# Optimization experiments

Hardware: AMD Instinct MI355X
Metric: run time of the kernel (lower is better)

Reference implementation:

```python
import jax, jax.numpy as jnp
import numpy as np

B, L, T = 64, 128, 48
E, HE, H = 512, 1024, 1024


def setup_inputs() -> dict:
    key = jax.random.key(0)
    ks = jax.random.split(key, 20)
    s = 0.02
    inp = {
        'enc_hiddens': jax.random.normal(ks[0], (B, L, HE), jnp.float32),
        'enc_masks': jax.random.randint(ks[1], (B, L), 0, 2, jnp.int32),
        'h1_init': jax.random.normal(ks[2], (B, H), jnp.float32),
        'c1_init': jax.random.normal(ks[3], (B, H), jnp.float32),
        'h2_init': jax.random.normal(ks[4], (B, H), jnp.float32),
        'c2_init': jax.random.normal(ks[5], (B, H), jnp.float32),
        'captions': jax.random.normal(ks[6], (T, B, E), jnp.float32),
        # LSTMCell 1: input E -> hidden H
        'W_ih1': jax.random.normal(ks[7], (4 * H, E), jnp.float32) * s,
        'W_hh1': jax.random.normal(ks[8], (4 * H, H), jnp.float32) * s,
        'b_ih1': jnp.zeros((4 * H,), jnp.float32),
        'b_hh1': jnp.zeros((4 * H,), jnp.float32),
        # LSTMCell 2: input 2H -> hidden H
        'W_ih2': jax.random.normal(ks[9], (4 * H, 2 * H), jnp.float32) * s,
        'W_hh2': jax.random.normal(ks[10], (4 * H, H), jnp.float32) * s,
        'b_ih2': jnp.zeros((4 * H,), jnp.float32),
        'b_hh2': jnp.zeros((4 * H,), jnp.float32),
        # att_projection: He -> H
        'W_att': jax.random.normal(ks[11], (H, HE), jnp.float32) * s,
        'b_att': jnp.zeros((H,), jnp.float32),
        # combined_output_projection: He+H -> H
        'W_comb': jax.random.normal(ks[12], (H, HE + H), jnp.float32) * s,
        'b_comb': jnp.zeros((H,), jnp.float32),
    }
    return inp


def _lstm_cell(x, h, c, W_ih, W_hh, b_ih, b_hh):
    gates = x @ W_ih.T + b_ih + h @ W_hh.T + b_hh  # (B, 4H)
    i, f, g, o = jnp.split(gates, 4, axis=-1)
    i = jax.nn.sigmoid(i)
    f = jax.nn.sigmoid(f)
    g = jnp.tanh(g)
    o = jax.nn.sigmoid(o)
    c_new = f * c + i * g
    h_new = o * jnp.tanh(c_new)
    return h_new, c_new


def reference(enc_hiddens, enc_masks, h1_init, c1_init, h2_init, c2_init, captions,
              W_ih1, W_hh1, b_ih1, b_hh1, W_ih2, W_hh2, b_ih2, b_hh2,
              W_att, b_att, W_comb, b_comb):
    # Precompute attention projection of encoder hiddens: (B, L, H)
    enc_proj = jnp.einsum('blf,hf->blh', enc_hiddens, W_att) + b_att
    mask = enc_masks.astype(bool)  # True -> masked with -inf
    o0 = jnp.zeros((enc_hiddens.shape[0], W_hh1.shape[1]), enc_hiddens.dtype)

    def step(carry, elem):
        h1, c1, h2, c2, o_prev = carry
        h1, c1 = _lstm_cell(elem, h1, c1, W_ih1, W_hh1, b_ih1, b_hh1)
        bar = jnp.concatenate([h1, o_prev], axis=1)  # (B, 2H)
        h2, c2 = _lstm_cell(bar, h2, c2, W_ih2, W_hh2, b_ih2, b_hh2)
        e_t = jnp.einsum('bh,blh->bl', h2, enc_proj)
        e_t = jnp.where(mask, -jnp.inf, e_t)
        alpha = jax.nn.softmax(e_t, axis=1)
        a_t = jnp.einsum('bl,blf->bf', alpha, enc_hiddens)  # (B, He)
        U_t = jnp.concatenate([a_t, h2], axis=1)
        o_t = jnp.tanh(U_t @ W_comb.T + b_comb)  # dropout is identity in eval
        return (h1, c1, h2, c2, o_t), o_t

    _, outs = jax.lax.scan(step, (h1_init, c1_init, h2_init, c2_init, o0), captions)
    return outs  # (T, B, H)
```

## Files before the change

kernel.cpp:

```cpp
#include <hip/hip_runtime.h>

static constexpr int Bn = 64, Ln = 128, Tn = 48, En = 512, HEn = 1024, Hn = 1024, Gn = 4096;

typedef _Float16 h16;
typedef __attribute__((ext_vector_type(8))) _Float16 h16x8;
typedef __attribute__((ext_vector_type(2))) _Float16 h16x2;
typedef __attribute__((ext_vector_type(4))) float f32x4;

__device__ __forceinline__ float sigf(float x){ return 1.f / (1.f + expf(-x)); }

__global__ void cvt2(const float* __restrict__ in, h16x2* __restrict__ out, int n2){
  int i = blockIdx.x * blockDim.x + threadIdx.x;
  int stride = gridDim.x * blockDim.x;
  for (; i < n2; i += stride){
    float2 v = reinterpret_cast<const float2*>(in)[i];
    h16x2 o; o.x = (h16)v.x; o.y = (h16)v.y;
    out[i] = o;
  }
}

__global__ void init_state(const float* __restrict__ h1i, const float* __restrict__ c1i,
                           const float* __restrict__ h2i, const float* __restrict__ c2i,
                           h16* __restrict__ h1a, float* __restrict__ c1,
                           h16* __restrict__ h2a, float* __restrict__ c2,
                           float* __restrict__ h2f, h16* __restrict__ oh){
  int i = blockIdx.x * blockDim.x + threadIdx.x;
  if (i < Bn * Hn){
    h1a[i] = (h16)h1i[i]; c1[i] = c1i[i];
    h2a[i] = (h16)h2i[i]; c2[i] = c2i[i];
    h2f[i] = h2i[i];
    oh[i] = (h16)0.f;
  }
}

__global__ __launch_bounds__(256, 2) void gemm_lds(
    const h16* __restrict__ A, int lda,
    const h16* __restrict__ Bw, int ldb,
    const float* __restrict__ bias0, const float* __restrict__ bias1,
    float* __restrict__ outF, h16* __restrict__ outH, int ldc, int K)
{
  __shared__ __align__(16) h16 sA[2][4096];
  __shared__ __align__(16) h16 sB[2][4096];
  int tid = threadIdx.x;
  int w = tid >> 6, lane = tid & 63;
  int la = lane & 15, q = lane >> 4;
  int wr = w >> 1, wc = w & 1;
  int m0 = blockIdx.x * 128, n0 = blockIdx.y * 128;

  int srow = tid >> 2, sq = tid & 3;
  const h16* gAa = A + (size_t)(m0 + srow) * lda + sq * 8;
  const h16* gAb = gAa + (size_t)64 * lda;
  const h16* gBa = Bw + (size_t)(n0 + srow) * ldb + sq * 8;
  const h16* gBb = gBa + (size_t)64 * ldb;
  int dO = sq * 1024 + srow * 8;

  f32x4 acc[4][4];
  #pragma unroll
  for (int i = 0; i < 4; i++)
    #pragma unroll
    for (int j = 0; j < 4; j++) acc[i][j] = (f32x4){0.f, 0.f, 0.f, 0.f};

  h16x8 rAa, rAb, rBa, rBb;
  auto GLOAD = [&](int kt){
    int k0 = kt * 32;
    rAa = *reinterpret_cast<const h16x8*>(gAa + k0);
    rAb = *reinterpret_cast<const h16x8*>(gAb + k0);
    rBa = *reinterpret_cast<const h16x8*>(gBa + k0);
    rBb = *reinterpret_cast<const h16x8*>(gBb + k0);
  };
  auto SWRITE = [&](int buf){
    *reinterpret_cast<h16x8*>(&sA[buf][dO])       = rAa;
    *reinterpret_cast<h16x8*>(&sA[buf][dO + 512]) = rAb;
    *reinterpret_cast<h16x8*>(&sB[buf][dO])       = rBa;
    *reinterpret_cast<h16x8*>(&sB[buf][dO + 512]) = rBb;
  };

  int NT = K / 32;
  GLOAD(0); SWRITE(0);
  GLOAD(1);
  __syncthreads();
  for (int t = 0; t < NT; t++){
    int buf = t & 1;
    h16x8 af[4], bf[4];
    #pragma unroll
    for (int mi = 0; mi < 4; mi++)
      af[mi] = *reinterpret_cast<const h16x8*>(&sA[buf][q * 1024 + (wr * 64 + mi * 16 + la) * 8]);
    #pragma unroll
    for (int ni = 0; ni < 4; ni++)
      bf[ni] = *reinterpret_cast<const h16x8*>(&sB[buf][q * 1024 + (wc * 64 + ni * 16 + la) * 8]);
    #pragma unroll
    for (int mi = 0; mi < 4; mi++)
      #pragma unroll
      for (int ni = 0; ni < 4; ni++)
        acc[mi][ni] = __builtin_amdgcn_mfma_f32_16x16x32_f16(af[mi], bf[ni], acc[mi][ni], 0, 0, 0);
    if (t + 1 < NT){
      __syncthreads();
      SWRITE((t + 1) & 1);
      if (t + 2 < NT) GLOAD(t + 2);
      __syncthreads();
    }
  }

  #pragma unroll
  for (int mi = 0; mi < 4; mi++){
    int mrow = m0 + wr * 64 + mi * 16 + q * 4;
    #pragma unroll
    for (int ni = 0; ni < 4; ni++){
      int n = n0 + wc * 64 + ni * 16 + la;
      float bs = (bias0 ? bias0[n] : 0.f) + (bias1 ? bias1[n] : 0.f);
      #pragma unroll
      for (int r = 0; r < 4; r++){
        float v = acc[mi][ni][r] + bs;
        size_t off = (size_t)(mrow + r) * ldc + n;
        if (outF) outF[off] = v;
        else      outH[off] = (h16)v;
      }
    }
  }
}

struct PBuf { h16x8 a0, a1, a2, a3, b; };

__device__ __forceinline__ void pld(PBuf& p, const h16* __restrict__ Ap,
                                    const h16* __restrict__ Bp, int k){
  p.a0 = *reinterpret_cast<const h16x8*>(Ap + k);
  p.a1 = *reinterpret_cast<const h16x8*>(Ap + 16 * Hn + k);
  p.a2 = *reinterpret_cast<const h16x8*>(Ap + 32 * Hn + k);
  p.a3 = *reinterpret_cast<const h16x8*>(Ap + 48 * Hn + k);
  p.b  = *reinterpret_cast<const h16x8*>(Bp + k);
}
__device__ __forceinline__ void pmm(const PBuf& p, f32x4* acc){
  acc[0] = __builtin_amdgcn_mfma_f32_16x16x32_f16(p.a0, p.b, acc[0], 0, 0, 0);
  acc[1] = __builtin_amdgcn_mfma_f32_16x16x32_f16(p.a1, p.b, acc[1], 0, 0, 0);
  acc[2] = __builtin_amdgcn_mfma_f32_16x16x32_f16(p.a2, p.b, acc[2], 0, 0, 0);
  acc[3] = __builtin_amdgcn_mfma_f32_16x16x32_f16(p.a3, p.b, acc[3], 0, 0, 0);
}

template<int NS>
__device__ __forceinline__ void gseg_pf(const h16* __restrict__ Ap,
                                        const h16* __restrict__ Bp, f32x4* acc){
  PBuf p0, p1, p2, p3;
  pld(p0, Ap, Bp, 0);
  pld(p1, Ap, Bp, 32);
  pld(p2, Ap, Bp, 64);
  pld(p3, Ap, Bp, 96);
  #pragma unroll 1
  for (int s = 0; s + 4 < NS; s += 4){
    pmm(p0, acc); pld(p0, Ap, Bp, (s + 4) * 32);
    pmm(p1, acc); pld(p1, Ap, Bp, (s + 5) * 32);
    pmm(p2, acc); pld(p2, Ap, Bp, (s + 6) * 32);
    pmm(p3, acc); pld(p3, Ap, Bp, (s + 7) * 32);
  }
  pmm(p0, acc); pmm(p1, acc); pmm(p2, acc); pmm(p3, acc);
}

struct PBuf2 { h16x8 a0, a1, b; };

__device__ __forceinline__ void pld2(PBuf2& p, const h16* __restrict__ Ap,
                                     const h16* __restrict__ Bp, int k){
  p.a0 = *reinterpret_cast<const h16x8*>(Ap + k);
  p.a1 = *reinterpret_cast<const h16x8*>(Ap + 16 * Hn + k);
  p.b  = *reinterpret_cast<const h16x8*>(Bp + k);
}
__device__ __forceinline__ void pmm2(const PBuf2& p, f32x4* acc){
  acc[0] = __builtin_amdgcn_mfma_f32_16x16x32_f16(p.a0, p.b, acc[0], 0, 0, 0);
  acc[1] = __builtin_amdgcn_mfma_f32_16x16x32_f16(p.a1, p.b, acc[1], 0, 0, 0);
}

template<int NS>
__device__ __forceinline__ void gseg2_pf(const h16* __restrict__ Ap,
                                         const h16* __restrict__ Bp, f32x4* acc){
  PBuf2 p0, p1, p2, p3;
  pld2(p0, Ap, Bp, 0);
  pld2(p1, Ap, Bp, 32);
  pld2(p2, Ap, Bp, 64);
  pld2(p3, Ap, Bp, 96);
  #pragma unroll 1
  for (int s = 0; s + 4 < NS; s += 4){
    pmm2(p0, acc); pld2(p0, Ap, Bp, (s + 4) * 32);
    pmm2(p1, acc); pld2(p1, Ap, Bp, (s + 5) * 32);
    pmm2(p2, acc); pld2(p2, Ap, Bp, (s + 6) * 32);
    pmm2(p3, acc); pld2(p3, Ap, Bp, (s + 7) * 32);
  }
  pmm2(p0, acc); pmm2(p1, acc); pmm2(p2, acc); pmm2(p3, acc);
}

__global__ __launch_bounds__(256, 2) void kA(
    const h16* __restrict__ h1cur, const h16* __restrict__ h2prev, const h16* __restrict__ oh,
    h16* __restrict__ h1next, h16* __restrict__ h2cur, float* __restrict__ h2f,
    float* __restrict__ c1, float* __restrict__ c2,
    const h16* __restrict__ wih2, const h16* __restrict__ whh2, const h16* __restrict__ whh1,
    const float* __restrict__ bih2, const float* __restrict__ bhh2,
    const float* __restrict__ pre1_t, int mode)
{
  __shared__ float sg[4][32][17];
  int bid = blockIdx.x, tid = threadIdx.x;
  int g = tid >> 6, lane = tid & 63;
  int la = lane & 15, q = lane >> 4;
  bool is2 = (mode == 1) && (bid < 128);
  int unit = is2 ? bid : (mode == 1 ? bid - 128 : bid);
  int jb = unit >> 1, mh = unit & 1;
  int j0 = jb * 16;
  int r0 = mh * 32;
  bool active = is2 || (pre1_t != nullptr);

  if (active){
    f32x4 acc[2];
    acc[0] = (f32x4){0.f, 0.f, 0.f, 0.f};
    acc[1] = (f32x4){0.f, 0.f, 0.f, 0.f};
    int n0 = g * 1024 + j0;
    const h16* Aoff;
    if (is2){
      gseg2_pf<32>(h1cur  + (size_t)(r0 + la) * Hn + q * 8,
                   wih2 + (size_t)(n0 + la) * 2048 + q * 8,        acc);
      gseg2_pf<32>(oh     + (size_t)(r0 + la) * Hn + q * 8,
                   wih2 + (size_t)(n0 + la) * 2048 + 1024 + q * 8, acc);
      gseg2_pf<32>(h2prev + (size_t)(r0 + la) * Hn + q * 8,
                   whh2 + (size_t)(n0 + la) * 1024 + q * 8,        acc);
    } else {
      gseg2_pf<32>(h1cur  + (size_t)(r0 + la) * Hn + q * 8,
                   whh1 + (size_t)(n0 + la) * 1024 + q * 8,        acc);
    }
    #pragma unroll
    for (int mi = 0; mi < 2; mi++)
      #pragma unroll
      for (int r = 0; r < 4; r++)
        sg[g][mi * 16 + q * 4 + r][la] = acc[mi][r];
  }
  __syncthreads();
  if (active){
    for (int e = tid; e < 512; e += 256){
      int rl = e >> 4, col = e & 15, j = j0 + col;
      int row = r0 + rl;
      float gi = sg[0][rl][col];
      float gf = sg[1][rl][col];
      float gg = sg[2][rl][col];
      float go = sg[3][rl][col];
      if (is2){
        gi += bih2[j] + bhh2[j];
        gf += bih2[j + 1024] + bhh2[j + 1024];
        gg += bih2[j + 2048] + bhh2[j + 2048];
        go += bih2[j + 3072] + bhh2[j + 3072];
        float c_ = sigf(gf) * c2[row * Hn + j] + sigf(gi) * tanhf(gg);
        c2[row * Hn + j] = c_;
        float h_ = sigf(go) * tanhf(c_);
        h2cur[row * Hn + j] = (h16)h_;
        h2f[row * Hn + j] = h_;
      } else {
        const float* p = pre1_t + (size_t)row * Gn;
        gi += p[j]; gf += p[j + 1024]; gg += p[j + 2048]; go += p[j + 3072];
        float c_ = sigf(gf) * c1[row * Hn + j] + sigf(gi) * tanhf(gg);
        c1[row * Hn + j] = c_;
        h1next[row * Hn + j] = (h16)(sigf(go) * tanhf(c_));
      }
    }
  }
}

__global__ __launch_bounds__(256, 2) void kB(
    const float* __restrict__ h2f, const h16* __restrict__ eph, const int* __restrict__ msk,
    float* __restrict__ ebuf,
    const h16* __restrict__ h2cur, const h16* __restrict__ wcomb, const float* __restrict__ bcomb,
    float* __restrict__ hwb)
{
  int bid = blockIdx.x, tid = threadIdx.x;
  int w = tid >> 6, lane = tid & 63;
  if (bid < 512){
    int wv = bid * 4 + w;
    int b = wv >> 5;
    int l0 = (wv & 31) * 4;
    const f32x4* h2r = reinterpret_cast<const f32x4*>(h2f + b * Hn + lane * 16);
    f32x4 hv0 = h2r[0], hv1 = h2r[1], hv2 = h2r[2], hv3 = h2r[3];
    #pragma unroll
    for (int li = 0; li < 4; li++){
      int l = l0 + li;
      const h16x8* er = reinterpret_cast<const h16x8*>(eph + ((size_t)b * Ln + l) * Hn + lane * 16);
      h16x8 e0 = er[0], e1 = er[1];
      float acc = 0.f;
      #pragma unroll
      for (int i = 0; i < 4; i++) acc += hv0[i] * (float)e0[i];
      #pragma unroll
      for (int i = 0; i < 4; i++) acc += hv1[i] * (float)e0[4 + i];
      #pragma unroll
      for (int i = 0; i < 4; i++) acc += hv2[i] * (float)e1[i];
      #pragma unroll
      for (int i = 0; i < 4; i++) acc += hv3[i] * (float)e1[4 + i];
      for (int off = 32; off; off >>= 1) acc += __shfl_xor(acc, off);
      if (lane == 0) ebuf[b * Ln + l] = msk[b * Ln + l] ? -1e30f : acc;
    }
  } else {
    int hb = bid - 512;
    int la = lane & 15, q = lane >> 4;
    int n0 = hb * 64 + w * 16;
    f32x4 acc[4];
    #pragma unroll
    for (int mi = 0; mi < 4; mi++) acc[mi] = (f32x4){0.f, 0.f, 0.f, 0.f};
    gseg_pf<32>(h2cur + la * Hn + q * 8,
                wcomb + (size_t)(n0 + la) * (HEn + Hn) + HEn + q * 8, acc);
    float bs = bcomb[n0 + la];
    #pragma unroll
    for (int mi = 0; mi < 4; mi++)
      #pragma unroll
      for (int r = 0; r < 4; r++)
        hwb[(size_t)(mi * 16 + q * 4 + r) * Hn + n0 + la] = acc[mi][r] + bs;
  }
}

__global__ __launch_bounds__(128, 4) void kC(
    int t, const float* __restrict__ ebuf,
    const h16* __restrict__ ecbh, const float* __restrict__ hwb,
    float* __restrict__ out, h16* __restrict__ oh)
{
  __shared__ float sb[Ln];
  __shared__ float red[4];
  int bid = blockIdx.x;
  int b = bid >> 2;
  int jq = (bid & 3) * 256;
  int tid = threadIdx.x;
  int w = tid >> 6;
  float e = ebuf[b * Ln + tid];
  float m = e;
  #pragma unroll
  for (int off = 32; off; off >>= 1) m = fmaxf(m, __shfl_xor(m, off));
  if ((tid & 63) == 0) red[w] = m;
  __syncthreads();
  m = fmaxf(red[0], red[1]);
  float ex = expf(e - m);
  sb[tid] = ex;
  float s = ex;
  #pragma unroll
  for (int off = 32; off; off >>= 1) s += __shfl_xor(s, off);
  if ((tid & 63) == 0) red[2 + w] = s;
  __syncthreads();
  float rinv = 1.f / (red[2] + red[3]);
  int j0 = jq + tid * 2;
  const h16* base = ecbh + (size_t)b * Ln * Hn + j0;
  float a0 = 0.f, a1 = 0.f, c0 = 0.f, c1 = 0.f;
  #pragma unroll 8
  for (int l = 0; l < Ln; l += 2){
    float al0 = sb[l], al1 = sb[l + 1];
    h16x2 p0 = *reinterpret_cast<const h16x2*>(base + (size_t)l * Hn);
    h16x2 p1 = *reinterpret_cast<const h16x2*>(base + (size_t)(l + 1) * Hn);
    a0 += al0 * (float)p0.x; a1 += al0 * (float)p0.y;
    c0 += al1 * (float)p1.x; c1 += al1 * (float)p1.y;
  }
  a0 = (a0 + c0) * rinv; a1 = (a1 + c1) * rinv;
  float2 hw2 = *reinterpret_cast<const float2*>(hwb + b * Hn + j0);
  float o0 = tanhf(a0 + hw2.x);
  float o1 = tanhf(a1 + hw2.y);
  *reinterpret_cast<float2*>(out + ((size_t)t * Bn + b) * Hn + j0) = make_float2(o0, o1);
  h16x2 opk; opk.x = (h16)o0; opk.y = (h16)o1;
  *reinterpret_cast<h16x2*>(oh + b * Hn + j0) = opk;
}

extern "C" void kernel_launch(void* const* d_in, const int* in_sizes, int n_in,
                              void* d_out, int out_size, void* d_ws, size_t ws_size,
                              hipStream_t stream)
{
  const float* enc   = (const float*)d_in[0];
  const int*   msk   = (const int*)  d_in[1];
  const float* h1i   = (const float*)d_in[2];
  const float* c1i   = (const float*)d_in[3];
  const float* h2i   = (const float*)d_in[4];
  const float* c2i   = (const float*)d_in[5];
  const float* caps  = (const float*)d_in[6];
  const float* Wih1  = (const float*)d_in[7];
  const float* Whh1  = (const float*)d_in[8];
  const float* bih1  = (const float*)d_in[9];
  const float* bhh1  = (const float*)d_in[10];
  const float* Wih2  = (const float*)d_in[11];
  const float* Whh2  = (const float*)d_in[12];
  const float* bih2  = (const float*)d_in[13];
  const float* bhh2  = (const float*)d_in[14];
  const float* Watt  = (const float*)d_in[15];
  const float* batt  = (const float*)d_in[16];
  const float* Wcomb = (const float*)d_in[17];
  const float* bcomb = (const float*)d_in[18];
  float* out = (float*)d_out;

  char* p = (char*)d_ws;
  auto take = [&](size_t bytes){ char* r = p; p += (bytes + 255) & ~(size_t)255; return r; };
  float* pre1   = (float*)take((size_t)Tn * Bn * Gn * 4);
  h16*   ench   = (h16*)take((size_t)Bn * Ln * HEn * 2);
  h16*   eph    = (h16*)take((size_t)Bn * Ln * Hn * 2);
  h16*   ecbh   = (h16*)take((size_t)Bn * Ln * Hn * 2);
  h16*   caph   = (h16*)take((size_t)Tn * Bn * En * 2);
  h16*   wih1h  = (h16*)take((size_t)Gn * En * 2);
  h16*   whh1h  = (h16*)take((size_t)Gn * Hn * 2);
  h16*   wih2h  = (h16*)take((size_t)Gn * 2 * Hn * 2);
  h16*   whh2h  = (h16*)take((size_t)Gn * Hn * 2);
  h16*   watth  = (h16*)take((size_t)Hn * HEn * 2);
  h16*   wcombh = (h16*)take((size_t)Hn * (HEn + Hn) * 2);
  h16*   h1b0   = (h16*)take((size_t)Bn * Hn * 2);
  h16*   h1b1   = (h16*)take((size_t)Bn * Hn * 2);
  h16*   h2b0   = (h16*)take((size_t)Bn * Hn * 2);
  h16*   h2b1   = (h16*)take((size_t)Bn * Hn * 2);
  h16*   oh     = (h16*)take((size_t)Bn * Hn * 2);
  float* c1     = (float*)take((size_t)Bn * Hn * 4);
  float* c2     = (float*)take((size_t)Bn * Hn * 4);
  float* h2f    = (float*)take((size_t)Bn * Hn * 4);
  float* ebuf   = (float*)take((size_t)Bn * Ln * 4);
  float* hwb    = (float*)take((size_t)Bn * Hn * 4);
  (void)ws_size; (void)n_in; (void)in_sizes; (void)out_size;

  auto cvt = [&](const float* src, void* dst, int n){
    int n2 = n / 2;
    int blocks = (n2 + 255) / 256; if (blocks > 2048) blocks = 2048;
    cvt2<<<blocks, 256, 0, stream>>>(src, (h16x2*)dst, n2);
  };
  cvt(enc,   ench,   Bn * Ln * HEn);
  cvt(caps,  caph,   Tn * Bn * En);
  cvt(Wih1,  wih1h,  Gn * En);
  cvt(Whh1,  whh1h,  Gn * Hn);
  cvt(Wih2,  wih2h,  Gn * 2 * Hn);
  cvt(Whh2,  whh2h,  Gn * Hn);
  cvt(Watt,  watth,  Hn * HEn);
  cvt(Wcomb, wcombh, Hn * (HEn + Hn));

  init_state<<<(Bn * Hn) / 256, 256, 0, stream>>>(h1i, c1i, h2i, c2i,
                                                  h1b0, c1, h2b0, c2, h2f, oh);

  gemm_lds<<<dim3((Tn * Bn) / 128, Gn / 128), 256, 0, stream>>>(
      caph, En, wih1h, En, bih1, bhh1, pre1, nullptr, Gn, En);
  gemm_lds<<<dim3((Bn * Ln) / 128, Hn / 128), 256, 0, stream>>>(
      ench, HEn, watth, HEn, batt, nullptr, nullptr, eph, Hn, HEn);
  gemm_lds<<<dim3((Bn * Ln) / 128, Hn / 128), 256, 0, stream>>>(
      ench, HEn, wcombh, HEn + Hn, nullptr, nullptr, nullptr, ecbh, Hn, HEn);

  kA<<<128, 256, 0, stream>>>(h1b0, h2b0, oh, h1b1, h2b1, h2f, c1, c2,
                              wih2h, whh2h, whh1h, bih2, bhh2, pre1, 0);

  h16* h1buf[2] = { h1b0, h1b1 };
  h16* h2buf[2] = { h2b0, h2b1 };
  for (int t = 0; t < Tn; t++){
    h16* h1cur  = h1buf[(t + 1) & 1];
    h16* h1next = h1buf[t & 1];
    h16* h2prev = h2buf[t & 1];
    h16* h2cur  = h2buf[(t + 1) & 1];
    const float* pre1_t = (t + 1 < Tn) ? (pre1 + (size_t)(t + 1) * Bn * Gn) : nullptr;
    kA<<<256, 256, 0, stream>>>(h1cur, h2prev, oh, h1next, h2cur, h2f, c1, c2,
                                wih2h, whh2h, whh1h, bih2, bhh2, pre1_t, 1);
    kB<<<528, 256, 0, stream>>>(h2f, eph, msk, ebuf, h2cur, wcombh, bcomb, hwb);
    kC<<<256, 128, 0, stream>>>(t, ebuf, ecbh, hwb, out, oh);
  }
}
```

Measured before the change: 3.290 ms.

## Split reduction work across more waves in the per-step LSTM, score and attention kernels

The per-timestep gate kernel now uses 512 threads per block and splits each GEMV's K dimension across two wave groups. The two partial results are summed in shared memory before the LSTM pointwise update. The score kernel gives each wave one encoder position instead of four, so it launches many more blocks, and the W_comb GEMV blocks now come first in the grid. The attention-context kernel splits the sequence dimension across two thread halves and combines them through shared memory. The aim is more parallelism and memory-level concurrency in these small, latency-bound per-step launches, at the cost of extra shared-memory reductions, an added barrier and lower occupancy per block.

Result: faster. 3.203 ms (-2.7%).

```diff
diff --git a/kernel.cpp b/kernel.cpp
--- a/kernel.cpp
+++ b/kernel.cpp
@@ -185,7 +185,7 @@
   pmm2(p0, acc); pmm2(p1, acc); pmm2(p2, acc); pmm2(p3, acc);
 }
 
-__global__ __launch_bounds__(256, 2) void kA(
+__global__ __launch_bounds__(512, 1) void kA(
     const h16* __restrict__ h1cur, const h16* __restrict__ h2prev, const h16* __restrict__ oh,
     h16* __restrict__ h1next, h16* __restrict__ h2cur, float* __restrict__ h2f,
     float* __restrict__ c1, float* __restrict__ c2,
@@ -193,9 +193,10 @@
     const float* __restrict__ bih2, const float* __restrict__ bhh2,
     const float* __restrict__ pre1_t, int mode)
 {
-  __shared__ float sg[4][32][17];
+  __shared__ float sg[4][2][32][17];
   int bid = blockIdx.x, tid = threadIdx.x;
-  int g = tid >> 6, lane = tid & 63;
+  int wv = tid >> 6, lane = tid & 63;
+  int g = wv & 3, kh = wv >> 2;
   int la = lane & 15, q = lane >> 4;
   bool is2 = (mode == 1) && (bid < 128);
   int unit = is2 ? bid : (mode == 1 ? bid - 128 : bid);
@@ -209,50 +210,52 @@
     acc[0] = (f32x4){0.f, 0.f, 0.f, 0.f};
     acc[1] = (f32x4){0.f, 0.f, 0.f, 0.f};
     int n0 = g * 1024 + j0;
-    const h16* Aoff;
+    size_t aoff = (size_t)(r0 + la) * Hn + q * 8;
     if (is2){
-      gseg2_pf<32>(h1cur  + (size_t)(r0 + la) * Hn + q * 8,
-                   wih2 + (size_t)(n0 + la) * 2048 + q * 8,        acc);
-      gseg2_pf<32>(oh     + (size_t)(r0 + la) * Hn + q * 8,
-                   wih2 + (size_t)(n0 + la) * 2048 + 1024 + q * 8, acc);
-      gseg2_pf<32>(h2prev + (size_t)(r0 + la) * Hn + q * 8,
-                   whh2 + (size_t)(n0 + la) * 1024 + q * 8,        acc);
+      if (kh == 0){
+        gseg2_pf<32>(h1cur + aoff, wih2 + (size_t)(n0 + la) * 2048 + q * 8,        acc);
+        gseg2_pf<16>(oh    + aoff, wih2 + (size_t)(n0 + la) * 2048 + 1024 + q * 8, acc);
+      } else {
+        gseg2_pf<16>(oh     + aoff + 512, wih2 + (size_t)(n0 + la) * 2048 + 1536 + q * 8, acc);
+        gseg2_pf<32>(h2prev + aoff,       whh2 + (size_t)(n0 + la) * 1024 + q * 8,        acc);
+      }
     } else {
-      gseg2_pf<32>(h1cur  + (size_t)(r0 + la) * Hn + q * 8,
-                   whh1 + (size_t)(n0 + la) * 1024 + q * 8,        acc);
+      if (kh == 0)
+        gseg2_pf<16>(h1cur + aoff,       whh1 + (size_t)(n0 + la) * 1024 + q * 8,       acc);
+      else
+        gseg2_pf<16>(h1cur + aoff + 512, whh1 + (size_t)(n0 + la) * 1024 + 512 + q * 8, acc);
     }
     #pragma unroll
     for (int mi = 0; mi < 2; mi++)
       #pragma unroll
       for (int r = 0; r < 4; r++)
-        sg[g][mi * 16 + q * 4 + r][la] = acc[mi][r];
+        sg[g][kh][mi * 16 + q * 4 + r][la] = acc[mi][r];
   }
   __syncthreads();
-  if (active){
-    for (int e = tid; e < 512; e += 256){
-      int rl = e >> 4, col = e & 15, j = j0 + col;
-      int row = r0 + rl;
-      float gi = sg[0][rl][col];
-      float gf = sg[1][rl][col];
-      float gg = sg[2][rl][col];
-      float go = sg[3][rl][col];
-      if (is2){
-        gi += bih2[j] + bhh2[j];
-        gf += bih2[j + 1024] + bhh2[j + 1024];
-        gg += bih2[j + 2048] + bhh2[j + 2048];
-        go += bih2[j + 3072] + bhh2[j + 3072];
-        float c_ = sigf(gf) * c2[row * Hn + j] + sigf(gi) * tanhf(gg);
-        c2[row * Hn + j] = c_;
-        float h_ = sigf(go) * tanhf(c_);
-        h2cur[row * Hn + j] = (h16)h_;
-        h2f[row * Hn + j] = h_;
-      } else {
-        const float* p = pre1_t + (size_t)row * Gn;
-        gi += p[j]; gf += p[j + 1024]; gg += p[j + 2048]; go += p[j + 3072];
-        float c_ = sigf(gf) * c1[row * Hn + j] + sigf(gi) * tanhf(gg);
-        c1[row * Hn + j] = c_;
-        h1next[row * Hn + j] = (h16)(sigf(go) * tanhf(c_));
-      }
+  if (active && tid < 512){
+    int e = tid;
+    int rl = e >> 4, col = e & 15, j = j0 + col;
+    int row = r0 + rl;
+    float gi = sg[0][0][rl][col] + sg[0][1][rl][col];
+    float gf = sg[1][0][rl][col] + sg[1][1][rl][col];
+    float gg = sg[2][0][rl][col] + sg[2][1][rl][col];
+    float go = sg[3][0][rl][col] + sg[3][1][rl][col];
+    if (is2){
+      gi += bih2[j] + bhh2[j];
+      gf += bih2[j + 1024] + bhh2[j + 1024];
+      gg += bih2[j + 2048] + bhh2[j + 2048];
+      go += bih2[j + 3072] + bhh2[j + 3072];
+      float c_ = sigf(gf) * c2[row * Hn + j] + sigf(gi) * tanhf(gg);
+      c2[row * Hn + j] = c_;
+      float h_ = sigf(go) * tanhf(c_);
+      h2cur[row * Hn + j] = (h16)h_;
+      h2f[row * Hn + j] = h_;
+    } else {
+      const float* p = pre1_t + (size_t)row * Gn;
+      gi += p[j]; gf += p[j + 1024]; gg += p[j + 2048]; go += p[j + 3072];
+      float c_ = sigf(gf) * c1[row * Hn + j] + sigf(gi) * tanhf(gg);
+      c1[row * Hn + j] = c_;
+      h1next[row * Hn + j] = (h16)(sigf(go) * tanhf(c_));
     }
   }
 }
@@ -265,31 +268,27 @@
 {
   int bid = blockIdx.x, tid = threadIdx.x;
   int w = tid >> 6, lane = tid & 63;
-  if (bid < 512){
-    int wv = bid * 4 + w;
-    int b = wv >> 5;
-    int l0 = (wv & 31) * 4;
-    const f32x4* h2r = reinterpret_cast<const f32x4*>(h2f + b * Hn + lane * 16);
+  if (bid >= 16){
+    int wv = (bid - 16) * 4 + w;
+    int b = wv >> 7;
+    int l = wv & 127;
+    const f32x4* h2r = reinterpret_cast<const f32x4*>(h2f + (size_t)b * Hn + lane * 16);
     f32x4 hv0 = h2r[0], hv1 = h2r[1], hv2 = h2r[2], hv3 = h2r[3];
-    #pragma unroll
-    for (int li = 0; li < 4; li++){
-      int l = l0 + li;
-      const h16x8* er = reinterpret_cast<const h16x8*>(eph + ((size_t)b * Ln + l) * Hn + lane * 16);
-      h16x8 e0 = er[0], e1 = er[1];
-      float acc = 0.f;
-      #pragma unroll
-      for (int i = 0; i < 4; i++) acc += hv0[i] * (float)e0[i];
-      #pragma unroll
-      for (int i = 0; i < 4; i++) acc += hv1[i] * (float)e0[4 + i];
-      #pragma unroll
-      for (int i = 0; i < 4; i++) acc += hv2[i] * (float)e1[i];
-      #pragma unroll
-      for (int i = 0; i < 4; i++) acc += hv3[i] * (float)e1[4 + i];
-      for (int off = 32; off; off >>= 1) acc += __shfl_xor(acc, off);
-      if (lane == 0) ebuf[b * Ln + l] = msk[b * Ln + l] ? -1e30f : acc;
-    }
+    const h16x8* er = reinterpret_cast<const h16x8*>(eph + ((size_t)b * Ln + l) * Hn + lane * 16);
+    h16x8 e0 = er[0], e1 = er[1];
+    float acc = 0.f;
+    #pragma unroll
+    for (int i = 0; i < 4; i++) acc += hv0[i] * (float)e0[i];
+    #pragma unroll
+    for (int i = 0; i < 4; i++) acc += hv1[i] * (float)e0[4 + i];
+    #pragma unroll
+    for (int i = 0; i < 4; i++) acc += hv2[i] * (float)e1[i];
+    #pragma unroll
+    for (int i = 0; i < 4; i++) acc += hv3[i] * (float)e1[4 + i];
+    for (int off = 32; off; off >>= 1) acc += __shfl_xor(acc, off);
+    if (lane == 0) ebuf[b * Ln + l] = msk[b * Ln + l] ? -1e30f : acc;
   } else {
-    int hb = bid - 512;
+    int hb = bid;
     int la = lane & 15, q = lane >> 4;
     int n0 = hb * 64 + w * 16;
     f32x4 acc[4];
@@ -306,51 +305,62 @@
   }
 }
 
-__global__ __launch_bounds__(128, 4) void kC(
+__global__ __launch_bounds__(256, 2) void kC(
     int t, const float* __restrict__ ebuf,
     const h16* __restrict__ ecbh, const float* __restrict__ hwb,
     float* __restrict__ out, h16* __restrict__ oh)
 {
   __shared__ float sb[Ln];
-  __shared__ float red[4];
+  __shared__ float rmax[4], rsum[4];
+  __shared__ float sp[128][2];
   int bid = blockIdx.x;
   int b = bid >> 2;
   int jq = (bid & 3) * 256;
   int tid = threadIdx.x;
-  int w = tid >> 6;
-  float e = ebuf[b * Ln + tid];
+  int wv = tid >> 6;
+  float e = ebuf[b * Ln + (tid & 127)];
   float m = e;
   #pragma unroll
   for (int off = 32; off; off >>= 1) m = fmaxf(m, __shfl_xor(m, off));
-  if ((tid & 63) == 0) red[w] = m;
+  if ((tid & 63) == 0) rmax[wv] = m;
   __syncthreads();
-  m = fmaxf(red[0], red[1]);
+  m = fmaxf(fmaxf(rmax[0], rmax[1]), fmaxf(rmax[2], rmax[3]));
   float ex = expf(e - m);
-  sb[tid] = ex;
+  if (tid < 128) sb[tid] = ex;
   float s = ex;
   #pragma unroll
   for (int off = 32; off; off >>= 1) s += __shfl_xor(s, off);
-  if ((tid & 63) == 0) red[2 + w] = s;
+  if ((tid & 63) == 0) rsum[wv] = s;
   __syncthreads();
-  float rinv = 1.f / (red[2] + red[3]);
-  int j0 = jq + tid * 2;
+  float rinv = 1.f / (rsum[0] + rsum[1]);
+
+  int col = tid & 127, lh = tid >> 7;
+  int j0 = jq + col * 2;
   const h16* base = ecbh + (size_t)b * Ln * Hn + j0;
   float a0 = 0.f, a1 = 0.f, c0 = 0.f, c1 = 0.f;
+  int lb = lh * 64;
   #pragma unroll 8
-  for (int l = 0; l < Ln; l += 2){
+  for (int i = 0; i < 64; i += 2){
+    int l = lb + i;
     float al0 = sb[l], al1 = sb[l + 1];
     h16x2 p0 = *reinterpret_cast<const h16x2*>(base + (size_t)l * Hn);
     h16x2 p1 = *reinterpret_cast<const h16x2*>(base + (size_t)(l + 1) * Hn);
     a0 += al0 * (float)p0.x; a1 += al0 * (float)p0.y;
     c0 += al1 * (float)p1.x; c1 += al1 * (float)p1.y;
   }
-  a0 = (a0 + c0) * rinv; a1 = (a1 + c1) * rinv;
-  float2 hw2 = *reinterpret_cast<const float2*>(hwb + b * Hn + j0);
-  float o0 = tanhf(a0 + hw2.x);
-  float o1 = tanhf(a1 + hw2.y);
-  *reinterpret_cast<float2*>(out + ((size_t)t * Bn + b) * Hn + j0) = make_float2(o0, o1);
-  h16x2 opk; opk.x = (h16)o0; opk.y = (h16)o1;
-  *reinterpret_cast<h16x2*>(oh + b * Hn + j0) = opk;
+  float t0 = a0 + c0, t1 = a1 + c1;
+  if (lh == 1){ sp[col][0] = t0; sp[col][1] = t1; }
+  __syncthreads();
+  if (lh == 0){
+    float g0 = (t0 + sp[col][0]) * rinv;
+    float g1 = (t1 + sp[col][1]) * rinv;
+    float2 hw2 = *reinterpret_cast<const float2*>(hwb + b * Hn + j0);
+    float o0 = tanhf(g0 + hw2.x);
+    float o1 = tanhf(g1 + hw2.y);
+    *reinterpret_cast<float2*>(out + ((size_t)t * Bn + b) * Hn + j0) = make_float2(o0, o1);
+    h16x2 opk; opk.x = (h16)o0; opk.y = (h16)o1;
+    *reinterpret_cast<h16x2*>(oh + (size_t)b * Hn + j0) = opk;
+  }
 }
 
 extern "C" void kernel_launch(void* const* d_in, const int* in_sizes, int n_in,
@@ -427,7 +437,7 @@
   gemm_lds<<<dim3((Bn * Ln) / 128, Hn / 128), 256, 0, stream>>>(
       ench, HEn, wcombh, HEn + Hn, nullptr, nullptr, nullptr, ecbh, Hn, HEn);
 
-  kA<<<128, 256, 0, stream>>>(h1b0, h2b0, oh, h1b1, h2b1, h2f, c1, c2,
+  kA<<<128, 512, 0, stream>>>(h1b0, h2b0, oh, h1b1, h2b1, h2f, c1, c2,
                               wih2h, whh2h, whh1h, bih2, bhh2, pre1, 0);
 
   h16* h1buf[2] = { h1b0, h1b1 };
@@ -438,9 +448,9 @@
     h16* h2prev = h2buf[t & 1];
     h16* h2cur  = h2buf[(t + 1) & 1];
     const float* pre1_t = (t + 1 < Tn) ? (pre1 + (size_t)(t + 1) * Bn * Gn) : nullptr;
-    kA<<<256, 256, 0, stream>>>(h1cur, h2prev, oh, h1next, h2cur, h2f, c1, c2,
+    kA<<<256, 512, 0, stream>>>(h1cur, h2prev, oh, h1next, h2cur, h2f, c1, c2,
                                 wih2h, whh2h, whh1h, bih2, bhh2, pre1_t, 1);
-    kB<<<528, 256, 0, stream>>>(h2f, eph, msk, ebuf, h2cur, wcombh, bcomb, hwb);
-    kC<<<256, 128, 0, stream>>>(t, ebuf, ecbh, hwb, out, oh);
-  }
-}
+    kB<<<2064, 256, 0, stream>>>(h2f, eph, msk, ebuf, h2cur, wcombh, bcomb, hwb);
+    kC<<<256, 256, 0, stream>>>(t, ebuf, ecbh, hwb, out, oh);
+  }
+}
```
